# Performance work log

Measured on AMD Instinct MI355X. Metric: run time of the kernel, lower is better.

## Reference

```python
import jax, jax.numpy as jnp
import numpy as np

N_NODES = 50000
N_EDGES = 800000
N_FEAT = 128
HIDDEN = 128
HEADS = 4
C = HIDDEN // HEADS  # per-head channels = 32
N_LAYERS = 3
OUT_DIM = 2048
N_GRAPHS = 1000
LEAKY = 0.2  # PyG GATConv default negative_slope


def setup_inputs() -> dict:
    key = jax.random.key(0)
    ks = jax.random.split(key, 12)
    x = jax.random.normal(ks[0], (N_NODES, N_FEAT), dtype=jnp.float32)
    edge_index = jax.random.randint(ks[1], (2, N_EDGES), 0, N_NODES, dtype=jnp.int32)
    edge_attr = jax.random.normal(ks[2], (N_EDGES, 1), dtype=jnp.float32)
    batch = (jnp.arange(N_NODES, dtype=jnp.int32) // (N_NODES // N_GRAPHS))  # 50 nodes per graph
    s = 1.0 / np.sqrt(HIDDEN)
    Ws = jax.random.normal(ks[3], (N_LAYERS, N_FEAT, HIDDEN), dtype=jnp.float32) * s
    att_src = jax.random.normal(ks[4], (N_LAYERS, HEADS, C), dtype=jnp.float32) * s
    att_dst = jax.random.normal(ks[5], (N_LAYERS, HEADS, C), dtype=jnp.float32) * s
    We = jax.random.normal(ks[6], (N_LAYERS, 1, HIDDEN), dtype=jnp.float32) * s
    att_e = jax.random.normal(ks[7], (N_LAYERS, HEADS, C), dtype=jnp.float32) * s
    biases = jnp.zeros((N_LAYERS, HIDDEN), dtype=jnp.float32)
    lin1_w = jax.random.normal(ks[8], (HIDDEN, OUT_DIM), dtype=jnp.float32) * s
    lin1_b = jnp.zeros((OUT_DIM,), dtype=jnp.float32)
    return {"x": x, "edge_index": edge_index, "edge_attr": edge_attr, "batch": batch,
            "Ws": Ws, "att_src": att_src, "att_dst": att_dst, "We": We,
            "att_e": att_e, "biases": biases, "lin1_w": lin1_w, "lin1_b": lin1_b}


def _gat_layer(x, src, dst, ea, W, a_s, a_d, We_l, a_e, b):
    """PyG GATConv: shared lin for src/dst, edge_dim=1, concat heads, eval mode."""
    N = x.shape[0]
    h = (x @ W).reshape(N, HEADS, C)                       # [N,H,C]
    al_s = jnp.einsum('nhc,hc->nh', h, a_s)                # [N,H]
    al_d = jnp.einsum('nhc,hc->nh', h, a_d)
    e = (ea @ We_l).reshape(-1, HEADS, C)                  # [E',H,C]
    al_e = jnp.einsum('ehc,hc->eh', e, a_e)
    logits = jax.nn.leaky_relu(al_s[src] + al_d[dst] + al_e, LEAKY)  # [E',H]
    # segment softmax over incoming edges of each dst node, per head
    m = jax.ops.segment_max(logits, dst, num_segments=N)
    m = jnp.where(jnp.isfinite(m), m, 0.0)
    ex = jnp.exp(logits - m[dst])
    den = jax.ops.segment_sum(ex, dst, num_segments=N)
    alpha = ex / (den[dst] + 1e-16)                        # [E',H]
    msg = alpha[:, :, None] * h[src]                       # [E',H,C]
    out = jax.ops.segment_sum(msg, dst, num_segments=N)    # [N,H,C]
    return out.reshape(N, HIDDEN) + b


def reference(x, edge_index, edge_attr, batch, Ws, att_src, att_dst, We, att_e, biases, lin1_w, lin1_b):
    N = x.shape[0]
    src, dst = edge_index[0], edge_index[1]
    # add_self_loops=True with fill_value='mean' (PyG default): self-loop
    # edge_attr at node i = mean of edge_attr over edges pointing to i.
    cnt = jax.ops.segment_sum(jnp.ones_like(edge_attr[:, 0]), dst, num_segments=N)
    ea_sum = jax.ops.segment_sum(edge_attr, dst, num_segments=N)
    ea_self = jnp.where(cnt[:, None] > 0, ea_sum / jnp.maximum(cnt[:, None], 1.0), 0.0)
    loop = jnp.arange(N, dtype=src.dtype)
    src_f = jnp.concatenate([src, loop])
    dst_f = jnp.concatenate([dst, loop])
    ea_f = jnp.concatenate([edge_attr, ea_self], axis=0)
    for l in range(N_LAYERS):
        x = _gat_layer(x, src_f, dst_f, ea_f, Ws[l], att_src[l], att_dst[l], We[l], att_e[l], biases[l])
        x = jax.nn.relu(x)  # dropout is identity in eval mode
    pooled = jax.ops.segment_max(x, batch, num_segments=N_GRAPHS, indices_are_sorted=True)
    out = pooled @ lin1_w + lin1_b
    return jax.nn.sigmoid(out)  # classes_is_bit=True
```

## Files before the change

### kernel.cpp

```cpp
#include <hip/hip_runtime.h>
#include <hip/hip_bf16.h>
#include <math.h>

#define NN 50000
#define NE 800000
#define HID 128
#define HEADS 4
#define CH 32
#define NG 1000
#define OUTD 2048
#define LEAKY 0.2f
#define NB196 ((NN + 255) / 256)

__device__ __forceinline__ float lrelu(float v) { return v >= 0.f ? v : LEAKY * v; }

__device__ __forceinline__ unsigned short f2bf(float f) {
    __hip_bfloat16 b = __float2bfloat16(f);
    return *reinterpret_cast<unsigned short*>(&b);
}
__device__ __forceinline__ float bflo(unsigned u) { return __uint_as_float(u << 16); }
__device__ __forceinline__ float bfhi(unsigned u) { return __uint_as_float(u & 0xffff0000u); }

__global__ void k_hist(const int* __restrict__ ei, int* __restrict__ deg,
                       int* __restrict__ pos) {
    int e = blockIdx.x * 256 + threadIdx.x;
    if (e >= NE) return;
    pos[e] = atomicAdd(&deg[ei[NE + e]], 1);
}

__global__ __launch_bounds__(256) void k_s1(const int* __restrict__ deg,
                                            int* __restrict__ loc,
                                            int* __restrict__ bsum) {
    __shared__ int ws[4];
    int t = blockIdx.x * 256 + threadIdx.x;
    int lane = threadIdx.x & 63, wid = threadIdx.x >> 6;
    int v = (t < NN) ? deg[t] : 0;
    int run = v;
    for (int off = 1; off < 64; off <<= 1) {
        int u = __shfl_up(run, off);
        if (lane >= off) run += u;
    }
    if (lane == 63) ws[wid] = run;
    __syncthreads();
    int wadd = 0;
    if (wid > 0) wadd += ws[0];
    if (wid > 1) wadd += ws[1];
    if (wid > 2) wadd += ws[2];
    if (t < NN) loc[t] = run - v + wadd;
    if (threadIdx.x == 255) bsum[blockIdx.x] = wadd + run;
}

__global__ __launch_bounds__(256) void k_s2(const int* __restrict__ bsum,
                                            int* __restrict__ bexcl) {
    __shared__ int ws[4];
    int t = threadIdx.x;
    int lane = t & 63, wid = t >> 6;
    int v = (t < NB196) ? bsum[t] : 0;
    int run = v;
    for (int off = 1; off < 64; off <<= 1) {
        int u = __shfl_up(run, off);
        if (lane >= off) run += u;
    }
    if (lane == 63) ws[wid] = run;
    __syncthreads();
    int wadd = 0;
    if (wid > 0) wadd += ws[0];
    if (wid > 1) wadd += ws[1];
    if (wid > 2) wadd += ws[2];
    if (t < NB196) bexcl[t] = run - v + wadd;
}

__global__ __launch_bounds__(256) void k_s3(const int* __restrict__ loc,
                                            const int* __restrict__ bexcl,
                                            int* __restrict__ rowptr) {
    int t = blockIdx.x * 256 + threadIdx.x;
    if (t < NN) rowptr[t] = loc[t] + bexcl[blockIdx.x];
    if (t == 0) rowptr[NN] = NE;
}

__global__ void k_scatter(const int* __restrict__ ei, const float* __restrict__ ea,
                          const int* __restrict__ rowptr, const int* __restrict__ pos,
                          int2* __restrict__ ep) {
    int e = blockIdx.x * 256 + threadIdx.x;
    if (e >= NE) return;
    int d = ei[NE + e];
    int2 rec;
    rec.x = ei[e];
    rec.y = __float_as_int(ea[e]);
    ep[rowptr[d] + pos[e]] = rec;
}

__global__ void k_coef(const float* __restrict__ We, const float* __restrict__ att_e,
                       float* __restrict__ coef) {
    int t = threadIdx.x;
    if (t < 12) {
        int l = t >> 2, hh = t & 3;
        const float* w = We + l * HID + hh * CH;
        const float* a = att_e + l * HID + hh * CH;
        float s = 0.f;
        for (int c = 0; c < CH; ++c) s += w[c] * a[c];
        coef[t] = s;
    }
}

__global__ __launch_bounds__(256) void k_gemm(const float* __restrict__ X,
                                              const float* __restrict__ W,
                                              const float* __restrict__ aw_s,
                                              const float* __restrict__ aw_d,
                                              unsigned short* __restrict__ H2,
                                              float* __restrict__ als,
                                              float* __restrict__ ald) {
    __shared__ float sW[HID * HID];
    __shared__ float sX[32 * HID];
    int t = threadIdx.x;
    int row0 = blockIdx.x * 32;
    for (int i = t; i < HID * HID / 4; i += 256)
        ((float4*)sW)[i] = ((const float4*)W)[i];
    for (int i = t; i < 32 * HID / 4; i += 256) {
        int r = i >> 5;
        int gr = row0 + r;
        float4 v = make_float4(0.f, 0.f, 0.f, 0.f);
        if (gr < NN) v = ((const float4*)X)[(size_t)gr * 32 + (i & 31)];
        ((float4*)sX)[i] = v;
    }
    int c0 = (t & 31) * 4;
    float4 as4 = *(const float4*)&aw_s[c0];
    float4 ad4 = *(const float4*)&aw_d[c0];
    __syncthreads();
    int r0 = (t >> 5) * 4;
    float4 a0 = make_float4(0,0,0,0), a1 = a0, a2 = a0, a3 = a0;
    for (int k = 0; k < HID; k += 4) {
        float4 w0 = *(const float4*)&sW[(k + 0) * HID + c0];
        float4 w1 = *(const float4*)&sW[(k + 1) * HID + c0];
        float4 w2 = *(const float4*)&sW[(k + 2) * HID + c0];
        float4 w3 = *(const float4*)&sW[(k + 3) * HID + c0];
        float4 x0 = *(const float4*)&sX[(r0 + 0) * HID + k];
        float4 x1 = *(const float4*)&sX[(r0 + 1) * HID + k];
        float4 x2 = *(const float4*)&sX[(r0 + 2) * HID + k];
        float4 x3 = *(const float4*)&sX[(r0 + 3) * HID + k];
        #define STEP(A, XV) \
            A.x += XV.x * w0.x + XV.y * w1.x + XV.z * w2.x + XV.w * w3.x; \
            A.y += XV.x * w0.y + XV.y * w1.y + XV.z * w2.y + XV.w * w3.y; \
            A.z += XV.x * w0.z + XV.y * w1.z + XV.z * w2.z + XV.w * w3.z; \
            A.w += XV.x * w0.w + XV.y * w1.w + XV.z * w2.w + XV.w * w3.w;
        STEP(a0, x0) STEP(a1, x1) STEP(a2, x2) STEP(a3, x3)
        #undef STEP
    }
    #define STORE(I, A) { int gr = row0 + r0 + I; if (gr < NN) { \
        ushort4 hb; hb.x = f2bf(A.x); hb.y = f2bf(A.y); \
        hb.z = f2bf(A.z); hb.w = f2bf(A.w); \
        *(ushort4*)&H2[(size_t)gr * HID + c0] = hb; } }
    STORE(0, a0) STORE(1, a1) STORE(2, a2) STORE(3, a3)
    #undef STORE
    float pa0 = a0.x*as4.x + a0.y*as4.y + a0.z*as4.z + a0.w*as4.w;
    float pa1 = a1.x*as4.x + a1.y*as4.y + a1.z*as4.z + a1.w*as4.w;
    float pa2 = a2.x*as4.x + a2.y*as4.y + a2.z*as4.z + a2.w*as4.w;
    float pa3 = a3.x*as4.x + a3.y*as4.y + a3.z*as4.z + a3.w*as4.w;
    float pd0 = a0.x*ad4.x + a0.y*ad4.y + a0.z*ad4.z + a0.w*ad4.w;
    float pd1 = a1.x*ad4.x + a1.y*ad4.y + a1.z*ad4.z + a1.w*ad4.w;
    float pd2 = a2.x*ad4.x + a2.y*ad4.y + a2.z*ad4.z + a2.w*ad4.w;
    float pd3 = a3.x*ad4.x + a3.y*ad4.y + a3.z*ad4.z + a3.w*ad4.w;
    for (int m = 1; m < 8; m <<= 1) {
        pa0 += __shfl_xor(pa0, m); pa1 += __shfl_xor(pa1, m);
        pa2 += __shfl_xor(pa2, m); pa3 += __shfl_xor(pa3, m);
        pd0 += __shfl_xor(pd0, m); pd1 += __shfl_xor(pd1, m);
        pd2 += __shfl_xor(pd2, m); pd3 += __shfl_xor(pd3, m);
    }
    if ((t & 7) == 0) {
        int h = (t & 31) >> 3;
        #define WR(I, PA, PD) { int gr = row0 + r0 + I; if (gr < NN) { \
            als[gr * 4 + h] = PA; ald[gr * 4 + h] = PD; } }
        WR(0, pa0, pd0) WR(1, pa1, pd1) WR(2, pa2, pd2) WR(3, pa3, pd3)
        #undef WR
    }
}

__global__ __launch_bounds__(256) void k_agg(const int* __restrict__ rowptr,
                                             const int2* __restrict__ ep,
                                             const float* __restrict__ als,
                                             const float* __restrict__ ald,
                                             const unsigned short* __restrict__ H2,
                                             const float* __restrict__ coef_l,
                                             const float* __restrict__ bias,
                                             float* __restrict__ out) {
    int n = blockIdx.x * 4 + (threadIdx.x >> 6);
    if (n >= NN) return;
    int lane = threadIdx.x & 63;
    int c = lane * 2;
    int h = lane >> 4;
    float coefh = coef_l[h];
    float aldh = ald[n * 4 + h];
    float s = 0.f, acc0 = 0.f, acc1 = 0.f, sum_ea = 0.f;
    int jb = rowptr[n], je = rowptr[n + 1];
    int j = jb;
    for (; j + 8 <= je; j += 8) {
        int2 e0 = ep[j],     e1 = ep[j + 1], e2 = ep[j + 2], e3 = ep[j + 3];
        int2 e4 = ep[j + 4], e5 = ep[j + 5], e6 = ep[j + 6], e7 = ep[j + 7];
        unsigned v0 = *(const unsigned*)&H2[(size_t)e0.x * HID + c];
        unsigned v1 = *(const unsigned*)&H2[(size_t)e1.x * HID + c];
        unsigned v2 = *(const unsigned*)&H2[(size_t)e2.x * HID + c];
        unsigned v3 = *(const unsigned*)&H2[(size_t)e3.x * HID + c];
        unsigned v4 = *(const unsigned*)&H2[(size_t)e4.x * HID + c];
        unsigned v5 = *(const unsigned*)&H2[(size_t)e5.x * HID + c];
        unsigned v6 = *(const unsigned*)&H2[(size_t)e6.x * HID + c];
        unsigned v7 = *(const unsigned*)&H2[(size_t)e7.x * HID + c];
        float l0 = als[e0.x * 4 + h], l1 = als[e1.x * 4 + h];
        float l2 = als[e2.x * 4 + h], l3 = als[e3.x * 4 + h];
        float l4 = als[e4.x * 4 + h], l5 = als[e5.x * 4 + h];
        float l6 = als[e6.x * 4 + h], l7 = als[e7.x * 4 + h];
        float a0 = __int_as_float(e0.y), a1 = __int_as_float(e1.y);
        float a2 = __int_as_float(e2.y), a3 = __int_as_float(e3.y);
        float a4 = __int_as_float(e4.y), a5 = __int_as_float(e5.y);
        float a6 = __int_as_float(e6.y), a7 = __int_as_float(e7.y);
        float p0 = __expf(lrelu(l0 + aldh + a0 * coefh));
        float p1 = __expf(lrelu(l1 + aldh + a1 * coefh));
        float p2 = __expf(lrelu(l2 + aldh + a2 * coefh));
        float p3 = __expf(lrelu(l3 + aldh + a3 * coefh));
        float p4 = __expf(lrelu(l4 + aldh + a4 * coefh));
        float p5 = __expf(lrelu(l5 + aldh + a5 * coefh));
        float p6 = __expf(lrelu(l6 + aldh + a6 * coefh));
        float p7 = __expf(lrelu(l7 + aldh + a7 * coefh));
        sum_ea += ((a0 + a1) + (a2 + a3)) + ((a4 + a5) + (a6 + a7));
        s += ((p0 + p1) + (p2 + p3)) + ((p4 + p5) + (p6 + p7));
        acc0 += p0 * bflo(v0) + p1 * bflo(v1);
        acc1 += p0 * bfhi(v0) + p1 * bfhi(v1);
        acc0 += p2 * bflo(v2) + p3 * bflo(v3);
        acc1 += p2 * bfhi(v2) + p3 * bfhi(v3);
        acc0 += p4 * bflo(v4) + p5 * bflo(v5);
        acc1 += p4 * bfhi(v4) + p5 * bfhi(v5);
        acc0 += p6 * bflo(v6) + p7 * bflo(v7);
        acc1 += p6 * bfhi(v6) + p7 * bfhi(v7);
    }
    for (; j < je; ++j) {
        int2 e0 = ep[j];
        float a0 = __int_as_float(e0.y);
        unsigned v0 = *(const unsigned*)&H2[(size_t)e0.x * HID + c];
        float p0 = __expf(lrelu(als[e0.x * 4 + h] + aldh + a0 * coefh));
        sum_ea += a0;
        s += p0;
        acc0 += p0 * bflo(v0);
        acc1 += p0 * bfhi(v0);
    }
    int degn = je - jb;
    float eaself = (degn > 0) ? sum_ea / (float)degn : 0.f;
    float ps = __expf(lrelu(als[n * 4 + h] + aldh + eaself * coefh));
    unsigned vs = *(const unsigned*)&H2[(size_t)n * HID + c];
    s += ps;
    acc0 += ps * bflo(vs);
    acc1 += ps * bfhi(vs);
    float inv = 1.0f / (s + 1e-16f);
    float2 o;
    o.x = fmaxf(acc0 * inv + bias[c], 0.f);
    o.y = fmaxf(acc1 * inv + bias[c + 1], 0.f);
    *(float2*)&out[(size_t)n * HID + c] = o;
}

__global__ void k_pool(const float* __restrict__ x, float* __restrict__ pooled) {
    int g = blockIdx.x;
    int c = threadIdx.x;
    float m = -INFINITY;
    const float* p = x + (size_t)g * 50 * HID + c;
    for (int i = 0; i < 50; ++i) m = fmaxf(m, p[i * HID]);
    pooled[g * HID + c] = m;
}

__global__ __launch_bounds__(256) void k_out(const float* __restrict__ pooled,
                                             const float* __restrict__ W,
                                             const float* __restrict__ b,
                                             float* __restrict__ out) {
    __shared__ float sp[8][HID];
    int t = threadIdx.x;
    int o = blockIdx.x * 256 + t;
    int g0 = blockIdx.y * 8;
    for (int i = t; i < 8 * HID / 4; i += 256)
        ((float4*)sp)[i] = ((const float4*)(pooled + (size_t)g0 * HID))[i];
    __syncthreads();
    float acc[8];
    #pragma unroll
    for (int g = 0; g < 8; ++g) acc[g] = 0.f;
    for (int k = 0; k < HID; ++k) {
        float wv = W[(size_t)k * OUTD + o];
        #pragma unroll
        for (int g = 0; g < 8; ++g) acc[g] += sp[g][k] * wv;
    }
    float bb = b[o];
    #pragma unroll
    for (int g = 0; g < 8; ++g)
        out[(size_t)(g0 + g) * OUTD + o] = 1.f / (1.f + expf(-(acc[g] + bb)));
}

extern "C" void kernel_launch(void* const* d_in, const int* in_sizes, int n_in,
                              void* d_out, int out_size, void* d_ws, size_t ws_size,
                              hipStream_t stream) {
    const float* x_in    = (const float*)d_in[0];
    const int*   ei      = (const int*)d_in[1];
    const float* ea      = (const float*)d_in[2];
    const float* Ws      = (const float*)d_in[4];
    const float* att_src = (const float*)d_in[5];
    const float* att_dst = (const float*)d_in[6];
    const float* We      = (const float*)d_in[7];
    const float* att_e   = (const float*)d_in[8];
    const float* biases  = (const float*)d_in[9];
    const float* lin1_w  = (const float*)d_in[10];
    const float* lin1_b  = (const float*)d_in[11];
    float* out = (float*)d_out;

    char* p = (char*)d_ws;
    int*   deg    = (int*)p;                 p += sizeof(int) * NN;
    int*   loc    = (int*)p;                 p += sizeof(int) * NN;
    int*   bsum   = (int*)p;                 p += sizeof(int) * 256;
    int*   bexcl  = (int*)p;                 p += sizeof(int) * 256;
    int*   rowptr = (int*)p;                 p += sizeof(int) * (NN + 1);
    p += sizeof(int) * 3;
    int*   pos    = (int*)p;                 p += sizeof(int) * NE;
    int2*  ep     = (int2*)p;                p += sizeof(int2) * NE;
    unsigned short* H2 = (unsigned short*)p; p += sizeof(short) * (size_t)NN * HID;
    float* xa     = (float*)p;               p += sizeof(float) * (size_t)NN * HID;
    float* xb     = (float*)p;               p += sizeof(float) * (size_t)NN * HID;
    float* als    = (float*)p;               p += sizeof(float) * NN * HEADS;
    float* ald    = (float*)p;               p += sizeof(float) * NN * HEADS;
    float* pooled = (float*)p;               p += sizeof(float) * NG * HID;
    float* coef   = (float*)p;               p += sizeof(float) * 12;

    hipMemsetAsync(deg, 0, sizeof(int) * NN, stream);
    k_hist<<<(NE + 255) / 256, 256, 0, stream>>>(ei, deg, pos);
    k_s1<<<NB196, 256, 0, stream>>>(deg, loc, bsum);
    k_s2<<<1, 256, 0, stream>>>(bsum, bexcl);
    k_s3<<<NB196, 256, 0, stream>>>(loc, bexcl, rowptr);
    k_scatter<<<(NE + 255) / 256, 256, 0, stream>>>(ei, ea, rowptr, pos, ep);
    k_coef<<<1, 64, 0, stream>>>(We, att_e, coef);

    for (int l = 0; l < 3; ++l) {
        const float* xin = (l == 0) ? x_in : (l == 1 ? xa : xb);
        float* xout      = (l == 1) ? xb : xa;
        k_gemm<<<1563, 256, 0, stream>>>(xin, Ws + (size_t)l * HID * HID,
                                         att_src + l * HEADS * CH,
                                         att_dst + l * HEADS * CH,
                                         H2, als, ald);
        k_agg<<<NN / 4, 256, 0, stream>>>(rowptr, ep, als, ald,
                                          H2, coef + l * 4, biases + l * HID, xout);
    }
    k_pool<<<NG, HID, 0, stream>>>(xa, pooled);
    dim3 og(OUTD / 256, NG / 8);
    k_out<<<og, 256, 0, stream>>>(pooled, lin1_w, lin1_b, out);
}
```

Measured before the change: 467.0 us.

## Use bf16 MFMA for layer GEMM and store activations in bf16

Replaces the fp32 shared-memory FMA GEMM with a bf16 MFMA 16x16x32 kernel that reads pre-converted bf16 inputs and transposed bf16 weights straight from global memory. The attention-logit dot products move into a separate small kernel that reads the bf16 H2. Layer outputs are now written as bf16 instead of fp32, which halves activation traffic for the next GEMM and for pooling. This adds two conversion kernels and one extra launch per layer, lowers precision of the intermediate activations, and computes als/ald from rounded bf16 values.

```diff
diff --git a/kernel.cpp b/kernel.cpp
--- a/kernel.cpp
+++ b/kernel.cpp
@@ -12,6 +12,9 @@
 #define LEAKY 0.2f
 #define NB196 ((NN + 255) / 256)
 
+typedef __attribute__((ext_vector_type(8))) short bshort8;
+typedef __attribute__((ext_vector_type(4))) float floatx4;
+
 __device__ __forceinline__ float lrelu(float v) { return v >= 0.f ? v : LEAKY * v; }
 
 __device__ __forceinline__ unsigned short f2bf(float f) {
@@ -20,6 +23,7 @@
 }
 __device__ __forceinline__ float bflo(unsigned u) { return __uint_as_float(u << 16); }
 __device__ __forceinline__ float bfhi(unsigned u) { return __uint_as_float(u & 0xffff0000u); }
+__device__ __forceinline__ float bfu(unsigned short u) { return __uint_as_float(((unsigned)u) << 16); }
 
 __global__ void k_hist(const int* __restrict__ ei, int* __restrict__ deg,
                        int* __restrict__ pos) {
@@ -103,76 +107,73 @@
     }
 }
 
-__global__ __launch_bounds__(256) void k_gemm(const float* __restrict__ X,
-                                              const float* __restrict__ W,
-                                              const float* __restrict__ aw_s,
-                                              const float* __restrict__ aw_d,
-                                              unsigned short* __restrict__ H2,
-                                              float* __restrict__ als,
-                                              float* __restrict__ ald) {
-    __shared__ float sW[HID * HID];
-    __shared__ float sX[32 * HID];
+__global__ void k_xcvt(const float* __restrict__ X, unsigned short* __restrict__ Xb) {
+    int t = blockIdx.x * 256 + threadIdx.x;
+    if (t >= NN * HID / 4) return;
+    float4 v = ((const float4*)X)[t];
+    ushort4 o;
+    o.x = f2bf(v.x); o.y = f2bf(v.y); o.z = f2bf(v.z); o.w = f2bf(v.w);
+    ((ushort4*)Xb)[t] = o;
+}
+
+__global__ void k_wt(const float* __restrict__ Ws, unsigned short* __restrict__ Wt) {
+    int t = blockIdx.x * 256 + threadIdx.x;
+    if (t >= 3 * HID * HID) return;
+    int l = t / (HID * HID), rem = t % (HID * HID);
+    int k = rem >> 7, n = rem & 127;
+    Wt[l * HID * HID + n * HID + k] = f2bf(Ws[l * HID * HID + k * HID + n]);
+}
+
+__global__ __launch_bounds__(256) void k_mm(const unsigned short* __restrict__ Xb,
+                                            const unsigned short* __restrict__ Wt,
+                                            unsigned short* __restrict__ H2) {
     int t = threadIdx.x;
-    int row0 = blockIdx.x * 32;
-    for (int i = t; i < HID * HID / 4; i += 256)
-        ((float4*)sW)[i] = ((const float4*)W)[i];
-    for (int i = t; i < 32 * HID / 4; i += 256) {
-        int r = i >> 5;
-        int gr = row0 + r;
-        float4 v = make_float4(0.f, 0.f, 0.f, 0.f);
-        if (gr < NN) v = ((const float4*)X)[(size_t)gr * 32 + (i & 31)];
-        ((float4*)sX)[i] = v;
-    }
-    int c0 = (t & 31) * 4;
-    float4 as4 = *(const float4*)&aw_s[c0];
-    float4 ad4 = *(const float4*)&aw_d[c0];
-    __syncthreads();
-    int r0 = (t >> 5) * 4;
-    float4 a0 = make_float4(0,0,0,0), a1 = a0, a2 = a0, a3 = a0;
-    for (int k = 0; k < HID; k += 4) {
-        float4 w0 = *(const float4*)&sW[(k + 0) * HID + c0];
-        float4 w1 = *(const float4*)&sW[(k + 1) * HID + c0];
-        float4 w2 = *(const float4*)&sW[(k + 2) * HID + c0];
-        float4 w3 = *(const float4*)&sW[(k + 3) * HID + c0];
-        float4 x0 = *(const float4*)&sX[(r0 + 0) * HID + k];
-        float4 x1 = *(const float4*)&sX[(r0 + 1) * HID + k];
-        float4 x2 = *(const float4*)&sX[(r0 + 2) * HID + k];
-        float4 x3 = *(const float4*)&sX[(r0 + 3) * HID + k];
-        #define STEP(A, XV) \
-            A.x += XV.x * w0.x + XV.y * w1.x + XV.z * w2.x + XV.w * w3.x; \
-            A.y += XV.x * w0.y + XV.y * w1.y + XV.z * w2.y + XV.w * w3.y; \
-            A.z += XV.x * w0.z + XV.y * w1.z + XV.z * w2.z + XV.w * w3.z; \
-            A.w += XV.x * w0.w + XV.y * w1.w + XV.z * w2.w + XV.w * w3.w;
-        STEP(a0, x0) STEP(a1, x1) STEP(a2, x2) STEP(a3, x3)
-        #undef STEP
-    }
-    #define STORE(I, A) { int gr = row0 + r0 + I; if (gr < NN) { \
-        ushort4 hb; hb.x = f2bf(A.x); hb.y = f2bf(A.y); \
-        hb.z = f2bf(A.z); hb.w = f2bf(A.w); \
-        *(ushort4*)&H2[(size_t)gr * HID + c0] = hb; } }
-    STORE(0, a0) STORE(1, a1) STORE(2, a2) STORE(3, a3)
-    #undef STORE
-    float pa0 = a0.x*as4.x + a0.y*as4.y + a0.z*as4.z + a0.w*as4.w;
-    float pa1 = a1.x*as4.x + a1.y*as4.y + a1.z*as4.z + a1.w*as4.w;
-    float pa2 = a2.x*as4.x + a2.y*as4.y + a2.z*as4.z + a2.w*as4.w;
-    float pa3 = a3.x*as4.x + a3.y*as4.y + a3.z*as4.z + a3.w*as4.w;
-    float pd0 = a0.x*ad4.x + a0.y*ad4.y + a0.z*ad4.z + a0.w*ad4.w;
-    float pd1 = a1.x*ad4.x + a1.y*ad4.y + a1.z*ad4.z + a1.w*ad4.w;
-    float pd2 = a2.x*ad4.x + a2.y*ad4.y + a2.z*ad4.z + a2.w*ad4.w;
-    float pd3 = a3.x*ad4.x + a3.y*ad4.y + a3.z*ad4.z + a3.w*ad4.w;
-    for (int m = 1; m < 8; m <<= 1) {
-        pa0 += __shfl_xor(pa0, m); pa1 += __shfl_xor(pa1, m);
-        pa2 += __shfl_xor(pa2, m); pa3 += __shfl_xor(pa3, m);
-        pd0 += __shfl_xor(pd0, m); pd1 += __shfl_xor(pd1, m);
-        pd2 += __shfl_xor(pd2, m); pd3 += __shfl_xor(pd3, m);
-    }
-    if ((t & 7) == 0) {
-        int h = (t & 31) >> 3;
-        #define WR(I, PA, PD) { int gr = row0 + r0 + I; if (gr < NN) { \
-            als[gr * 4 + h] = PA; ald[gr * 4 + h] = PD; } }
-        WR(0, pa0, pd0) WR(1, pa1, pd1) WR(2, pa2, pd2) WR(3, pa3, pd3)
-        #undef WR
-    }
+    int wv = t >> 6, lane = t & 63;
+    int m0 = blockIdx.x * 64 + wv * 16;
+    int ln = lane & 15, kg = lane >> 4;
+    int row = m0 + ln;
+    int rc = row < NN ? row : NN - 1;
+    floatx4 acc[8];
+    #pragma unroll
+    for (int nt = 0; nt < 8; ++nt) acc[nt] = (floatx4){0.f, 0.f, 0.f, 0.f};
+    #pragma unroll
+    for (int kc = 0; kc < HID; kc += 32) {
+        bshort8 a = *(const bshort8*)&Xb[rc * HID + kc + kg * 8];
+        #pragma unroll
+        for (int nt = 0; nt < 8; ++nt) {
+            bshort8 b = *(const bshort8*)&Wt[(nt * 16 + ln) * HID + kc + kg * 8];
+            acc[nt] = __builtin_amdgcn_mfma_f32_16x16x32_bf16(a, b, acc[nt], 0, 0, 0);
+        }
+    }
+    #pragma unroll
+    for (int nt = 0; nt < 8; ++nt) {
+        #pragma unroll
+        for (int r = 0; r < 4; ++r) {
+            int ro = m0 + kg * 4 + r;
+            if (ro < NN) H2[ro * HID + nt * 16 + ln] = f2bf(acc[nt][r]);
+        }
+    }
+}
+
+__global__ void k_al(const unsigned short* __restrict__ H2,
+                     const float* __restrict__ aw_s, const float* __restrict__ aw_d,
+                     float* __restrict__ als, float* __restrict__ ald) {
+    int t = blockIdx.x * 256 + threadIdx.x;
+    if (t >= NN * HEADS) return;
+    int n = t >> 2, h = t & 3;
+    const unsigned* hw = (const unsigned*)(H2 + n * HID + h * CH);
+    const float* sw = aw_s + h * CH;
+    const float* dw = aw_d + h * CH;
+    float s = 0.f, d = 0.f;
+    #pragma unroll
+    for (int i = 0; i < 16; ++i) {
+        unsigned u = hw[i];
+        float v0 = bflo(u), v1 = bfhi(u);
+        s += v0 * sw[2 * i] + v1 * sw[2 * i + 1];
+        d += v0 * dw[2 * i] + v1 * dw[2 * i + 1];
+    }
+    als[t] = s;
+    ald[t] = d;
 }
 
 __global__ __launch_bounds__(256) void k_agg(const int* __restrict__ rowptr,
@@ -182,12 +183,13 @@
                                              const unsigned short* __restrict__ H2,
                                              const float* __restrict__ coef_l,
                                              const float* __restrict__ bias,
-                                             float* __restrict__ out) {
+                                             unsigned short* __restrict__ xout) {
     int n = blockIdx.x * 4 + (threadIdx.x >> 6);
     if (n >= NN) return;
     int lane = threadIdx.x & 63;
     int c = lane * 2;
     int h = lane >> 4;
+    const unsigned* H2w = (const unsigned*)H2;
     float coefh = coef_l[h];
     float aldh = ald[n * 4 + h];
     float s = 0.f, acc0 = 0.f, acc1 = 0.f, sum_ea = 0.f;
@@ -196,14 +198,14 @@
     for (; j + 8 <= je; j += 8) {
         int2 e0 = ep[j],     e1 = ep[j + 1], e2 = ep[j + 2], e3 = ep[j + 3];
         int2 e4 = ep[j + 4], e5 = ep[j + 5], e6 = ep[j + 6], e7 = ep[j + 7];
-        unsigned v0 = *(const unsigned*)&H2[(size_t)e0.x * HID + c];
-        unsigned v1 = *(const unsigned*)&H2[(size_t)e1.x * HID + c];
-        unsigned v2 = *(const unsigned*)&H2[(size_t)e2.x * HID + c];
-        unsigned v3 = *(const unsigned*)&H2[(size_t)e3.x * HID + c];
-        unsigned v4 = *(const unsigned*)&H2[(size_t)e4.x * HID + c];
-        unsigned v5 = *(const unsigned*)&H2[(size_t)e5.x * HID + c];
-        unsigned v6 = *(const unsigned*)&H2[(size_t)e6.x * HID + c];
-        unsigned v7 = *(const unsigned*)&H2[(size_t)e7.x * HID + c];
+        unsigned v0 = H2w[e0.x * 64 + lane];
+        unsigned v1 = H2w[e1.x * 64 + lane];
+        unsigned v2 = H2w[e2.x * 64 + lane];
+        unsigned v3 = H2w[e3.x * 64 + lane];
+        unsigned v4 = H2w[e4.x * 64 + lane];
+        unsigned v5 = H2w[e5.x * 64 + lane];
+        unsigned v6 = H2w[e6.x * 64 + lane];
+        unsigned v7 = H2w[e7.x * 64 + lane];
         float l0 = als[e0.x * 4 + h], l1 = als[e1.x * 4 + h];
         float l2 = als[e2.x * 4 + h], l3 = als[e3.x * 4 + h];
         float l4 = als[e4.x * 4 + h], l5 = als[e5.x * 4 + h];
@@ -234,7 +236,7 @@
     for (; j < je; ++j) {
         int2 e0 = ep[j];
         float a0 = __int_as_float(e0.y);
-        unsigned v0 = *(const unsigned*)&H2[(size_t)e0.x * HID + c];
+        unsigned v0 = H2w[e0.x * 64 + lane];
         float p0 = __expf(lrelu(als[e0.x * 4 + h] + aldh + a0 * coefh));
         sum_ea += a0;
         s += p0;
@@ -244,23 +246,25 @@
     int degn = je - jb;
     float eaself = (degn > 0) ? sum_ea / (float)degn : 0.f;
     float ps = __expf(lrelu(als[n * 4 + h] + aldh + eaself * coefh));
-    unsigned vs = *(const unsigned*)&H2[(size_t)n * HID + c];
+    unsigned vs = H2w[n * 64 + lane];
     s += ps;
     acc0 += ps * bflo(vs);
     acc1 += ps * bfhi(vs);
     float inv = 1.0f / (s + 1e-16f);
-    float2 o;
-    o.x = fmaxf(acc0 * inv + bias[c], 0.f);
-    o.y = fmaxf(acc1 * inv + bias[c + 1], 0.f);
-    *(float2*)&out[(size_t)n * HID + c] = o;
-}
-
-__global__ void k_pool(const float* __restrict__ x, float* __restrict__ pooled) {
+    float o0 = fmaxf(acc0 * inv + bias[c], 0.f);
+    float o1 = fmaxf(acc1 * inv + bias[c + 1], 0.f);
+    ushort2 ov;
+    ov.x = f2bf(o0);
+    ov.y = f2bf(o1);
+    *(ushort2*)&xout[n * HID + c] = ov;
+}
+
+__global__ void k_pool(const unsigned short* __restrict__ x, float* __restrict__ pooled) {
     int g = blockIdx.x;
     int c = threadIdx.x;
     float m = -INFINITY;
-    const float* p = x + (size_t)g * 50 * HID + c;
-    for (int i = 0; i < 50; ++i) m = fmaxf(m, p[i * HID]);
+    const unsigned short* p = x + g * 50 * HID + c;
+    for (int i = 0; i < 50; ++i) m = fmaxf(m, bfu(p[i * HID]));
     pooled[g * HID + c] = m;
 }
 
@@ -273,20 +277,20 @@
     int o = blockIdx.x * 256 + t;
     int g0 = blockIdx.y * 8;
     for (int i = t; i < 8 * HID / 4; i += 256)
-        ((float4*)sp)[i] = ((const float4*)(pooled + (size_t)g0 * HID))[i];
+        ((float4*)sp)[i] = ((const float4*)(pooled + g0 * HID))[i];
     __syncthreads();
     float acc[8];
     #pragma unroll
     for (int g = 0; g < 8; ++g) acc[g] = 0.f;
     for (int k = 0; k < HID; ++k) {
-        float wv = W[(size_t)k * OUTD + o];
+        float wv = W[k * OUTD + o];
         #pragma unroll
         for (int g = 0; g < 8; ++g) acc[g] += sp[g][k] * wv;
     }
     float bb = b[o];
     #pragma unroll
     for (int g = 0; g < 8; ++g)
-        out[(size_t)(g0 + g) * OUTD + o] = 1.f / (1.f + expf(-(acc[g] + bb)));
+        out[(g0 + g) * OUTD + o] = 1.f / (1.f + expf(-(acc[g] + bb)));
 }
 
 extern "C" void kernel_launch(void* const* d_in, const int* in_sizes, int n_in,
@@ -314,9 +318,11 @@
     p += sizeof(int) * 3;
     int*   pos    = (int*)p;                 p += sizeof(int) * NE;
     int2*  ep     = (int2*)p;                p += sizeof(int2) * NE;
-    unsigned short* H2 = (unsigned short*)p; p += sizeof(short) * (size_t)NN * HID;
-    float* xa     = (float*)p;               p += sizeof(float) * (size_t)NN * HID;
-    float* xb     = (float*)p;               p += sizeof(float) * (size_t)NN * HID;
+    unsigned short* H2  = (unsigned short*)p; p += sizeof(short) * (size_t)NN * HID;
+    unsigned short* Xb0 = (unsigned short*)p; p += sizeof(short) * (size_t)NN * HID;
+    unsigned short* xa  = (unsigned short*)p; p += sizeof(short) * (size_t)NN * HID;
+    unsigned short* xb  = (unsigned short*)p; p += sizeof(short) * (size_t)NN * HID;
+    unsigned short* Wt  = (unsigned short*)p; p += sizeof(short) * 3 * HID * HID;
     float* als    = (float*)p;               p += sizeof(float) * NN * HEADS;
     float* ald    = (float*)p;               p += sizeof(float) * NN * HEADS;
     float* pooled = (float*)p;               p += sizeof(float) * NG * HID;
@@ -329,14 +335,15 @@
     k_s3<<<NB196, 256, 0, stream>>>(loc, bexcl, rowptr);
     k_scatter<<<(NE + 255) / 256, 256, 0, stream>>>(ei, ea, rowptr, pos, ep);
     k_coef<<<1, 64, 0, stream>>>(We, att_e, coef);
+    k_wt<<<(3 * HID * HID + 255) / 256, 256, 0, stream>>>(Ws, Wt);
+    k_xcvt<<<(NN * HID / 4 + 255) / 256, 256, 0, stream>>>(x_in, Xb0);
 
     for (int l = 0; l < 3; ++l) {
-        const float* xin = (l == 0) ? x_in : (l == 1 ? xa : xb);
-        float* xout      = (l == 1) ? xb : xa;
-        k_gemm<<<1563, 256, 0, stream>>>(xin, Ws + (size_t)l * HID * HID,
-                                         att_src + l * HEADS * CH,
-                                         att_dst + l * HEADS * CH,
-                                         H2, als, ald);
+        const unsigned short* xin = (l == 0) ? Xb0 : (l == 1 ? xa : xb);
+        unsigned short* xout      = (l == 1) ? xb : xa;
+        k_mm<<<(NN + 63) / 64, 256, 0, stream>>>(xin, Wt + l * HID * HID, H2);
+        k_al<<<(NN * HEADS + 255) / 256, 256, 0, stream>>>(
+            H2, att_src + l * HEADS * CH, att_dst + l * HEADS * CH, als, ald);
         k_agg<<<NN / 4, 256, 0, stream>>>(rowptr, ep, als, ald,
                                           H2, coef + l * 4, biases + l * HID, xout);
     }
```

Result: faster. 435.5 us (-6.7%).
